# Kernel optimization log

Measured on AMD Instinct MI355X. Metric: run time of the kernel, lower is better.

## Reference

```python
import jax, jax.numpy as jnp
import numpy as np

B, T, N_EMBD, N_HEAD, HEAD_DIM = 4, 2048, 32, 8, 4


def rxtx_blocks(X):
    """Vectorized faithful port of rxtx_4x4 over blocks. X: [..., 4, 4] -> C: [..., 4, 4].
    Computes clip(X) @ clip(X)^T via the 26-multiplication RXTX formulas, except the
    (0,0) and (3,3) entries are 0 (the source sets s1..s8 = 0). Output clipped to [-100,100]."""
    X = jnp.clip(X, -100.0, 100.0)
    (X1, X2, X3, X4) = (X[..., 0, 0], X[..., 0, 1], X[..., 0, 2], X[..., 0, 3])
    (X5, X6, X7, X8) = (X[..., 1, 0], X[..., 1, 1], X[..., 1, 2], X[..., 1, 3])
    (X9, X10, X11, X12) = (X[..., 2, 0], X[..., 2, 1], X[..., 2, 2], X[..., 2, 3])
    (X13, X14, X15, X16) = (X[..., 3, 0], X[..., 3, 1], X[..., 3, 2], X[..., 3, 3])
    m1 = (-X2 + X3 - X4 + X8) * (X8 + X11)
    m2 = (X1 - X5 - X6 + X7) * (X15 + X5)
    m3 = (-X2 + X12) * (-X10 + X16 + X12)
    m4 = (X9 - X6) * (X13 + X9 - X14)
    m5 = (X2 + X11) * (-X6 + X15 - X7)
    m6 = (X6 + X11) * (X6 + X7 - X11)
    m7 = X11 * (X6 + X7)
    m8 = X2 * (-X14 - X10 + X6 - X15 + X7 + X16 + X12)
    m9 = X6 * (X13 + X9 - X14 - X10 + X6 + X7 - X11)
    m10 = (X2 - X3 + X7 + X11 + X4 - X8) * X11
    m11 = (X5 + X6 - X7) * X5
    m12 = (X2 - X3 + X4) * X8
    m13 = (-X1 + X5 + X6 + X3 - X7 + X11) * X15
    m14 = (-X1 + X5 + X6) * (X13 + X9 + X15)
    m15 = (X2 + X4 - X8) * (X11 + X16 + X12)
    m16 = (X1 - X8) * (X9 - X16)
    m17 = X12 * (X10 - X12)
    m18 = X9 * (X13 - X14)
    m19 = (-X2 + X3) * (-X15 + X7 + X8)
    m20 = (X5 + X9 - X8) * X9
    m21 = X8 * (X9 - X8 + X12)
    m22 = (-X6 + X7) * (X5 + X7 - X11)
    m23 = X1 * (X13 - X5 + X16)
    m24 = (-X1 + X4 + X12) * X16
    m25 = (X9 + X2 + X10) * X14
    m26 = (X6 + X10 + X12) * X10
    z1 = m7 - m11 - m12
    z2 = m1 + m12 + m21
    z3 = m3 + m17 - m24
    z4 = m2 + m11 + m23
    z5 = m5 + m7 + m8
    z6 = m4 - m18 - m20
    z7 = m6 - m7 - m9
    z8 = m17 + m18
    c01 = m2 - m5 - z1 + m13 + m19
    c02 = z2 + z3 + m15 + m16
    c03 = z4 - z3 - z5 - m13
    c11 = m1 + m6 - z1 + m10 + m22
    c12 = z2 - z6 + z7 + m10
    c13 = z4 + z6 + m14 + m16
    c22 = m4 - z7 - z8 + m26
    c23 = m3 + z5 + z8 + m25
    zero = jnp.zeros_like(X1)  # s1..s8 = 0 in the source -> corner diagonals are 0
    row0 = jnp.stack([zero, c01, c02, c03], axis=-1)
    row1 = jnp.stack([c01, c11, c12, c13], axis=-1)
    row2 = jnp.stack([c02, c12, c22, c23], axis=-1)
    row3 = jnp.stack([c03, c13, c23, zero], axis=-1)
    C = jnp.stack([row0, row1, row2, row3], axis=-2)
    return jnp.clip(C, -100.0, 100.0)


def setup_inputs() -> dict:
    key = jax.random.key(0)
    ks = jax.random.split(key, 9)
    w_std = 0.02  # ~ xavier_uniform with gain=0.1 for 32x32
    x = jax.random.normal(ks[0], (B, T, N_EMBD), dtype=jnp.float32)
    Wq = jax.random.normal(ks[1], (N_EMBD, N_EMBD), dtype=jnp.float32) * w_std
    Wk = jax.random.normal(ks[2], (N_EMBD, N_EMBD), dtype=jnp.float32) * w_std
    Wv = jax.random.normal(ks[3], (N_EMBD, N_EMBD), dtype=jnp.float32) * w_std
    Wp = jax.random.normal(ks[4], (N_EMBD, N_EMBD), dtype=jnp.float32) * w_std
    bq = jnp.zeros((N_EMBD,), jnp.float32)
    bk = jnp.zeros((N_EMBD,), jnp.float32)
    bv = jnp.zeros((N_EMBD,), jnp.float32)
    bp = jnp.zeros((N_EMBD,), jnp.float32)
    return {"x": x, "Wq": Wq, "bq": bq, "Wk": Wk, "bk": bk, "Wv": Wv, "bv": bv, "Wp": Wp, "bp": bp}


def reference(x, Wq, bq, Wk, bk, Wv, bv, Wp, bp):
    Bx, Tx, Cx = x.shape  # T divisible by 4 -> no padding branch
    H, hd = N_HEAD, HEAD_DIM
    q = (x @ Wq.T + bq).reshape(Bx, Tx, H, hd).transpose(0, 2, 1, 3)  # [B,H,T,4]
    k = (x @ Wk.T + bk)  # computed in the original module but never used in scores
    v = (x @ Wv.T + bv).reshape(Bx, Tx, H, hd).transpose(0, 2, 1, 3)  # [B,H,T,4]
    nb = Tx // 4
    Cb = rxtx_blocks(q.reshape(Bx, H, nb, 4, 4))  # [B,H,nb,4,4]
    # scores[b,h, i*4+r, j*4+c] = Cb[b,h,i,r,c] for every j (source ignores k_block)
    scores = jnp.broadcast_to(Cb[:, :, :, :, None, :], (Bx, H, nb, 4, nb, 4)).reshape(Bx, H, Tx, Tx)
    scores = jnp.clip(scores, -100.0, 100.0) / jnp.sqrt(jnp.float32(hd))
    attn = jax.nn.softmax(scores, axis=-1)  # dropout is identity in eval mode
    out = jnp.einsum('bhts,bhsd->bhtd', attn, v)
    out = out.transpose(0, 2, 1, 3).reshape(Bx, Tx, Cx)
    return out @ Wp.T + bp
```

## Files before the change

### kernel.cpp

```cpp
#include <hip/hip_runtime.h>
#include <math.h>

#define TT 2048
#define CE 32

__device__ __forceinline__ float clip100(float v) {
    return fminf(fmaxf(v, -100.f), 100.f);
}

__device__ __forceinline__ float4 shfl_xor4(float4 v, int m) {
    float4 r;
    r.x = __shfl_xor(v.x, m, 64);
    r.y = __shfl_xor(v.y, m, 64);
    r.z = __shfl_xor(v.z, m, 64);
    r.w = __shfl_xor(v.w, m, 64);
    return r;
}

__global__ __launch_bounds__(512, 2) void k_fused(const float* __restrict__ x,
        const float* __restrict__ Wq, const float* __restrict__ bq,
        const float* __restrict__ Wv, const float* __restrict__ bv,
        const float* __restrict__ Wp, const float* __restrict__ bp,
        float* __restrict__ out) {
    int blk = blockIdx.x;
    int b   = blk >> 6;
    int t0  = (blk & 63) * 32;
    int tid = threadIdx.x;
    int tl  = tid >> 4;
    int h   = (tid >> 1) & 7;
    int s   = tid & 1;

    __shared__ float xs[32][33];
    __shared__ float wqs[32][33];
    __shared__ float wvs[32][33];
    __shared__ float wps[32][33];
    __shared__ float pbuf[32][36];
    __shared__ float Zl[32][36];
    __shared__ float xavg[4][33];
    __shared__ float4 red4[16][32];
    __shared__ float bqs[32], bvs[32], bps[32];

    if (tid < 256) {
        int rr = tid >> 3, cq = tid & 7;
        *reinterpret_cast<float4*>(&wqs[rr][cq * 4]) =
            *reinterpret_cast<const float4*>(Wq + rr * 32 + cq * 4);
        *reinterpret_cast<float4*>(&wvs[rr][cq * 4]) =
            *reinterpret_cast<const float4*>(Wv + rr * 32 + cq * 4);
        *reinterpret_cast<float4*>(&wps[rr][cq * 4]) =
            *reinterpret_cast<const float4*>(Wp + rr * 32 + cq * 4);
    } else {
        int u = tid - 256;
        int r2 = u >> 3, q2 = u & 7;
        *reinterpret_cast<float4*>(&xs[r2][q2 * 4]) =
            *reinterpret_cast<const float4*>(x + ((size_t)b * TT + t0 + r2) * CE + q2 * 4);
        if (u < 32)      bqs[u] = bq[u];
        else if (u < 64) bvs[u - 32] = bv[u - 32];
        else if (u < 96) bps[u - 64] = bp[u - 64];
    }

    {
        const float4* xb4 = reinterpret_cast<const float4*>(x + (size_t)b * TT * CE);
        float4 acc; acc.x = 0.f; acc.y = 0.f; acc.z = 0.f; acc.w = 0.f;
#pragma unroll 8
        for (int it = 0; it < 32; ++it) {
            float4 v = xb4[tid + 512 * it];
            acc.x += v.x; acc.y += v.y; acc.z += v.z; acc.w += v.w;
        }
        red4[tid >> 5][tid & 31] = acc;
    }
    __syncthreads();

    if (tid < 128) {
        int c = tid >> 5, e = tid & 31;
        int g = c * 8 + (e >> 2), comp = e & 3;
        float sm = 0.f;
#pragma unroll
        for (int rg = 0; rg < 16; ++rg)
            sm += reinterpret_cast<const float*>(&red4[rg][g])[comp];
        xavg[c][e] = sm * (1.f / 512.f);
    }

    float4 myq;
    {
        float a0 = 0.f, a1 = 0.f, a2 = 0.f, a3 = 0.f;
#pragma unroll
        for (int e4 = 0; e4 < 4; ++e4) {
            int e = s * 16 + e4 * 4;
            float4 xv = *reinterpret_cast<const float4*>(&xs[tl][e]);
            float4 w0 = *reinterpret_cast<const float4*>(&wqs[4 * h + 0][e]);
            float4 w1 = *reinterpret_cast<const float4*>(&wqs[4 * h + 1][e]);
            float4 w2 = *reinterpret_cast<const float4*>(&wqs[4 * h + 2][e]);
            float4 w3 = *reinterpret_cast<const float4*>(&wqs[4 * h + 3][e]);
            a0 += xv.x * w0.x + xv.y * w0.y + xv.z * w0.z + xv.w * w0.w;
            a1 += xv.x * w1.x + xv.y * w1.y + xv.z * w1.z + xv.w * w1.w;
            a2 += xv.x * w2.x + xv.y * w2.y + xv.z * w2.z + xv.w * w2.w;
            a3 += xv.x * w3.x + xv.y * w3.y + xv.z * w3.z + xv.w * w3.w;
        }
        myq.x = clip100(bqs[4 * h + 0] + a0 + __shfl_xor(a0, 1, 64));
        myq.y = clip100(bqs[4 * h + 1] + a1 + __shfl_xor(a1, 1, 64));
        myq.z = clip100(bqs[4 * h + 2] + a2 + __shfl_xor(a2, 1, 64));
        myq.w = clip100(bqs[4 * h + 3] + a3 + __shfl_xor(a3, 1, 64));
    }

    {
        int r = tl & 3;
        float4 q16 = shfl_xor4(myq, 16);
        float4 q32 = shfl_xor4(myq, 32);
        float4 q48 = shfl_xor4(myq, 48);
        float4 R0 = (r == 0) ? myq : (r == 1) ? q16 : (r == 2) ? q32 : q48;
        float4 R1 = (r == 1) ? myq : (r == 0) ? q16 : (r == 3) ? q32 : q48;
        float4 R2 = (r == 2) ? myq : (r == 3) ? q16 : (r == 0) ? q32 : q48;
        float4 R3 = (r == 3) ? myq : (r == 2) ? q16 : (r == 1) ? q32 : q48;

        float X1 = R0.x, X2 = R0.y, X3 = R0.z, X4 = R0.w;
        float X5 = R1.x, X6 = R1.y, X7 = R1.z, X8 = R1.w;
        float X9 = R2.x, X10 = R2.y, X11 = R2.z, X12 = R2.w;
        float X13 = R3.x, X14 = R3.y, X15 = R3.z, X16 = R3.w;

        float m1  = (-X2 + X3 - X4 + X8) * (X8 + X11);
        float m2  = (X1 - X5 - X6 + X7) * (X15 + X5);
        float m3  = (-X2 + X12) * (-X10 + X16 + X12);
        float m4  = (X9 - X6) * (X13 + X9 - X14);
        float m5  = (X2 + X11) * (-X6 + X15 - X7);
        float m6  = (X6 + X11) * (X6 + X7 - X11);
        float m7  = X11 * (X6 + X7);
        float m8  = X2 * (-X14 - X10 + X6 - X15 + X7 + X16 + X12);
        float m9  = X6 * (X13 + X9 - X14 - X10 + X6 + X7 - X11);
        float m10 = (X2 - X3 + X7 + X11 + X4 - X8) * X11;
        float m11 = (X5 + X6 - X7) * X5;
        float m12 = (X2 - X3 + X4) * X8;
        float m13 = (-X1 + X5 + X6 + X3 - X7 + X11) * X15;
        float m14 = (-X1 + X5 + X6) * (X13 + X9 + X15);
        float m15 = (X2 + X4 - X8) * (X11 + X16 + X12);
        float m16 = (X1 - X8) * (X9 - X16);
        float m17 = X12 * (X10 - X12);
        float m18 = X9 * (X13 - X14);
        float m19 = (-X2 + X3) * (-X15 + X7 + X8);
        float m20 = (X5 + X9 - X8) * X9;
        float m21 = X8 * (X9 - X8 + X12);
        float m22 = (-X6 + X7) * (X5 + X7 - X11);
        float m23 = X1 * (X13 - X5 + X16);
        float m24 = (-X1 + X4 + X12) * X16;
        float m25 = (X9 + X2 + X10) * X14;
        float m26 = (X6 + X10 + X12) * X10;
        float z1 = m7 - m11 - m12;
        float z2 = m1 + m12 + m21;
        float z3 = m3 + m17 - m24;
        float z4 = m2 + m11 + m23;
        float z5 = m5 + m7 + m8;
        float z6 = m4 - m18 - m20;
        float z7 = m6 - m7 - m9;
        float z8 = m17 + m18;
        float c01 = m2 - m5 - z1 + m13 + m19;
        float c02 = z2 + z3 + m15 + m16;
        float c03 = z4 - z3 - z5 - m13;
        float c11 = m1 + m6 - z1 + m10 + m22;
        float c12 = z2 - z6 + z7 + m10;
        float c13 = z4 + z6 + m14 + m16;
        float c22 = m4 - z7 - z8 + m26;
        float c23 = m3 + z5 + z8 + m25;

        float g0, g1, g2, g3;
        if (r == 0)      { g0 = 0.f; g1 = c01; g2 = c02; g3 = c03; }
        else if (r == 1) { g0 = c01; g1 = c11; g2 = c12; g3 = c13; }
        else if (r == 2) { g0 = c02; g1 = c12; g2 = c22; g3 = c23; }
        else             { g0 = c03; g1 = c13; g2 = c23; g3 = 0.f; }
        g0 = clip100(g0) * 0.5f; g1 = clip100(g1) * 0.5f;
        g2 = clip100(g2) * 0.5f; g3 = clip100(g3) * 0.5f;

        float mx = fmaxf(fmaxf(g0, g1), fmaxf(g2, g3));
        float p0 = __expf(g0 - mx), p1 = __expf(g1 - mx);
        float p2 = __expf(g2 - mx), p3 = __expf(g3 - mx);
        float inv = 1.f / (p0 + p1 + p2 + p3);
        if (s == 0) {
            float4 pv; pv.x = p0 * inv; pv.y = p1 * inv;
            pv.z = p2 * inv; pv.w = p3 * inv;
            *reinterpret_cast<float4*>(&pbuf[tl][4 * h]) = pv;
        }
    }
    __syncthreads();

    {
        int k  = tid >> 4;
        int oq = (tid >> 1) & 7;
        int sh = tid & 1;
        int h2 = k >> 2, c2 = k & 3;
        float vv0 = 0.f, vv1 = 0.f, vv2 = 0.f, vv3 = 0.f;
#pragma unroll
        for (int e4 = 0; e4 < 4; ++e4) {
            int e = sh * 16 + e4 * 4;
            float xa0 = xavg[c2][e + 0];
            float xa1 = xavg[c2][e + 1];
            float xa2 = xavg[c2][e + 2];
            float xa3 = xavg[c2][e + 3];
            float4 w0 = *reinterpret_cast<const float4*>(&wvs[4 * h2 + 0][e]);
            float4 w1 = *reinterpret_cast<const float4*>(&wvs[4 * h2 + 1][e]);
            float4 w2 = *reinterpret_cast<const float4*>(&wvs[4 * h2 + 2][e]);
            float4 w3 = *reinterpret_cast<const float4*>(&wvs[4 * h2 + 3][e]);
            vv0 += xa0 * w0.x + xa1 * w0.y + xa2 * w0.z + xa3 * w0.w;
            vv1 += xa0 * w1.x + xa1 * w1.y + xa2 * w1.z + xa3 * w1.w;
            vv2 += xa0 * w2.x + xa1 * w2.y + xa2 * w2.z + xa3 * w2.w;
            vv3 += xa0 * w3.x + xa1 * w3.y + xa2 * w3.z + xa3 * w3.w;
        }
        vv0 = bvs[4 * h2 + 0] + vv0 + __shfl_xor(vv0, 1, 64);
        vv1 = bvs[4 * h2 + 1] + vv1 + __shfl_xor(vv1, 1, 64);
        vv2 = bvs[4 * h2 + 2] + vv2 + __shfl_xor(vv2, 1, 64);
        vv3 = bvs[4 * h2 + 3] + vv3 + __shfl_xor(vv3, 1, 64);
        float zz[2];
#pragma unroll
        for (int dd2 = 0; dd2 < 2; ++dd2) {
            int dd = 2 * sh + dd2;
            float4 wp = *reinterpret_cast<const float4*>(&wps[4 * oq + dd][4 * h2]);
            zz[dd2] = vv0 * wp.x + vv1 * wp.y + vv2 * wp.z + vv3 * wp.w;
        }
        float2 z2v; z2v.x = zz[0]; z2v.y = zz[1];
        *reinterpret_cast<float2*>(&Zl[k][4 * oq + 2 * sh]) = z2v;
    }
    __syncthreads();

    {
        int j = h;
        float o0 = 0.f, o1 = 0.f, o2 = 0.f, o3 = 0.f;
#pragma unroll
        for (int k4 = 0; k4 < 4; ++k4) {
            float4 pv = *reinterpret_cast<const float4*>(&pbuf[tl][16 * s + 4 * k4]);
#pragma unroll
            for (int kk = 0; kk < 4; ++kk) {
                float p = ((const float*)&pv)[kk];
                float4 zv = *reinterpret_cast<const float4*>(&Zl[16 * s + 4 * k4 + kk][4 * j]);
                o0 += p * zv.x; o1 += p * zv.y; o2 += p * zv.z; o3 += p * zv.w;
            }
        }
        o0 += __shfl_xor(o0, 1, 64); o1 += __shfl_xor(o1, 1, 64);
        o2 += __shfl_xor(o2, 1, 64); o3 += __shfl_xor(o3, 1, 64);
        if (s == 0) {
            float4 ov;
            ov.x = bps[4 * j + 0] + o0; ov.y = bps[4 * j + 1] + o1;
            ov.z = bps[4 * j + 2] + o2; ov.w = bps[4 * j + 3] + o3;
            float* orow = out + ((size_t)b * TT + t0 + tl) * CE;
            *reinterpret_cast<float4*>(orow + 4 * j) = ov;
        }
    }
}

extern "C" void kernel_launch(void* const* d_in, const int* in_sizes, int n_in,
                              void* d_out, int out_size, void* d_ws, size_t ws_size,
                              hipStream_t stream) {
    const float* x  = (const float*)d_in[0];
    const float* Wq = (const float*)d_in[1];
    const float* bq = (const float*)d_in[2];
    const float* Wv = (const float*)d_in[5];
    const float* bv = (const float*)d_in[6];
    const float* Wp = (const float*)d_in[7];
    const float* bp = (const float*)d_in[8];
    float* out = (float*)d_out;

    hipLaunchKernelGGL(k_fused, dim3(256), dim3(512), 0, stream,
                       x, Wq, bq, Wv, bv, Wp, bp, out);
}
```

Baseline: 12.39 us.

## Split warps: half reduce column means while other half computes q and softmax

Threads are specialized by role. Threads 256-511 now run the full batch-sum reduction over x, with twice as many iterations each. Threads 0-255 compute the q projection without a pair split (one thread per row-head), then the RXTX scores and softmax, with the shuffle offsets changed to match the new lane mapping. The goal is to overlap the memory-bound reduction with the compute-bound q/softmax stage. The cost is an extra __syncthreads and a longer serial load loop per reducing thread.

```diff
diff --git a/kernel.cpp b/kernel.cpp
--- a/kernel.cpp
+++ b/kernel.cpp
@@ -26,9 +26,6 @@
     int b   = blk >> 6;
     int t0  = (blk & 63) * 32;
     int tid = threadIdx.x;
-    int tl  = tid >> 4;
-    int h   = (tid >> 1) & 7;
-    int s   = tid & 1;
 
     __shared__ float xs[32][33];
     __shared__ float wqs[32][33];
@@ -37,7 +34,7 @@
     __shared__ float pbuf[32][36];
     __shared__ float Zl[32][36];
     __shared__ float xavg[4][33];
-    __shared__ float4 red4[16][32];
+    __shared__ float4 red4[8][32];
     __shared__ float bqs[32], bvs[32], bps[32];
 
     if (tid < 256) {
@@ -48,69 +45,55 @@
             *reinterpret_cast<const float4*>(Wv + rr * 32 + cq * 4);
         *reinterpret_cast<float4*>(&wps[rr][cq * 4]) =
             *reinterpret_cast<const float4*>(Wp + rr * 32 + cq * 4);
+        if (tid < 32)       bqs[tid] = bq[tid];
+        else if (tid < 64)  bvs[tid - 32] = bv[tid - 32];
+        else if (tid < 96)  bps[tid - 64] = bp[tid - 64];
     } else {
         int u = tid - 256;
         int r2 = u >> 3, q2 = u & 7;
         *reinterpret_cast<float4*>(&xs[r2][q2 * 4]) =
             *reinterpret_cast<const float4*>(x + ((size_t)b * TT + t0 + r2) * CE + q2 * 4);
-        if (u < 32)      bqs[u] = bq[u];
-        else if (u < 64) bvs[u - 32] = bv[u - 32];
-        else if (u < 96) bps[u - 64] = bp[u - 64];
-    }
-
-    {
+    }
+    __syncthreads();
+
+    if (tid >= 256) {
+        int u = tid - 256;
         const float4* xb4 = reinterpret_cast<const float4*>(x + (size_t)b * TT * CE);
         float4 acc; acc.x = 0.f; acc.y = 0.f; acc.z = 0.f; acc.w = 0.f;
-#pragma unroll 8
-        for (int it = 0; it < 32; ++it) {
-            float4 v = xb4[tid + 512 * it];
+#pragma unroll 16
+        for (int it = 0; it < 64; ++it) {
+            float4 v = xb4[u + 256 * it];
             acc.x += v.x; acc.y += v.y; acc.z += v.z; acc.w += v.w;
         }
-        red4[tid >> 5][tid & 31] = acc;
-    }
-    __syncthreads();
-
-    if (tid < 128) {
-        int c = tid >> 5, e = tid & 31;
-        int g = c * 8 + (e >> 2), comp = e & 3;
-        float sm = 0.f;
-#pragma unroll
-        for (int rg = 0; rg < 16; ++rg)
-            sm += reinterpret_cast<const float*>(&red4[rg][g])[comp];
-        xavg[c][e] = sm * (1.f / 512.f);
-    }
-
-    float4 myq;
-    {
-        float a0 = 0.f, a1 = 0.f, a2 = 0.f, a3 = 0.f;
-#pragma unroll
-        for (int e4 = 0; e4 < 4; ++e4) {
-            int e = s * 16 + e4 * 4;
-            float4 xv = *reinterpret_cast<const float4*>(&xs[tl][e]);
-            float4 w0 = *reinterpret_cast<const float4*>(&wqs[4 * h + 0][e]);
-            float4 w1 = *reinterpret_cast<const float4*>(&wqs[4 * h + 1][e]);
-            float4 w2 = *reinterpret_cast<const float4*>(&wqs[4 * h + 2][e]);
-            float4 w3 = *reinterpret_cast<const float4*>(&wqs[4 * h + 3][e]);
+        red4[u >> 5][u & 31] = acc;
+    } else {
+        int tl = tid >> 3, h = tid & 7;
+        float a0 = bqs[4 * h + 0], a1 = bqs[4 * h + 1];
+        float a2 = bqs[4 * h + 2], a3 = bqs[4 * h + 3];
+#pragma unroll
+        for (int e4 = 0; e4 < 8; ++e4) {
+            float4 xv = *reinterpret_cast<const float4*>(&xs[tl][e4 * 4]);
+            float4 w0 = *reinterpret_cast<const float4*>(&wqs[4 * h + 0][e4 * 4]);
+            float4 w1 = *reinterpret_cast<const float4*>(&wqs[4 * h + 1][e4 * 4]);
+            float4 w2 = *reinterpret_cast<const float4*>(&wqs[4 * h + 2][e4 * 4]);
+            float4 w3 = *reinterpret_cast<const float4*>(&wqs[4 * h + 3][e4 * 4]);
             a0 += xv.x * w0.x + xv.y * w0.y + xv.z * w0.z + xv.w * w0.w;
             a1 += xv.x * w1.x + xv.y * w1.y + xv.z * w1.z + xv.w * w1.w;
             a2 += xv.x * w2.x + xv.y * w2.y + xv.z * w2.z + xv.w * w2.w;
             a3 += xv.x * w3.x + xv.y * w3.y + xv.z * w3.z + xv.w * w3.w;
         }
-        myq.x = clip100(bqs[4 * h + 0] + a0 + __shfl_xor(a0, 1, 64));
-        myq.y = clip100(bqs[4 * h + 1] + a1 + __shfl_xor(a1, 1, 64));
-        myq.z = clip100(bqs[4 * h + 2] + a2 + __shfl_xor(a2, 1, 64));
-        myq.w = clip100(bqs[4 * h + 3] + a3 + __shfl_xor(a3, 1, 64));
-    }
-
-    {
+        float4 myq;
+        myq.x = clip100(a0); myq.y = clip100(a1);
+        myq.z = clip100(a2); myq.w = clip100(a3);
+
         int r = tl & 3;
+        float4 q8  = shfl_xor4(myq, 8);
         float4 q16 = shfl_xor4(myq, 16);
-        float4 q32 = shfl_xor4(myq, 32);
-        float4 q48 = shfl_xor4(myq, 48);
-        float4 R0 = (r == 0) ? myq : (r == 1) ? q16 : (r == 2) ? q32 : q48;
-        float4 R1 = (r == 1) ? myq : (r == 0) ? q16 : (r == 3) ? q32 : q48;
-        float4 R2 = (r == 2) ? myq : (r == 3) ? q16 : (r == 0) ? q32 : q48;
-        float4 R3 = (r == 3) ? myq : (r == 2) ? q16 : (r == 1) ? q32 : q48;
+        float4 q24 = shfl_xor4(myq, 24);
+        float4 R0 = (r == 0) ? myq : (r == 1) ? q8 : (r == 2) ? q16 : q24;
+        float4 R1 = (r == 1) ? myq : (r == 0) ? q8 : (r == 3) ? q16 : q24;
+        float4 R2 = (r == 2) ? myq : (r == 3) ? q8 : (r == 0) ? q16 : q24;
+        float4 R3 = (r == 3) ? myq : (r == 2) ? q8 : (r == 1) ? q16 : q24;
 
         float X1 = R0.x, X2 = R0.y, X3 = R0.z, X4 = R0.w;
         float X5 = R1.x, X6 = R1.y, X7 = R1.z, X8 = R1.w;
@@ -172,11 +155,20 @@
         float p0 = __expf(g0 - mx), p1 = __expf(g1 - mx);
         float p2 = __expf(g2 - mx), p3 = __expf(g3 - mx);
         float inv = 1.f / (p0 + p1 + p2 + p3);
-        if (s == 0) {
-            float4 pv; pv.x = p0 * inv; pv.y = p1 * inv;
-            pv.z = p2 * inv; pv.w = p3 * inv;
-            *reinterpret_cast<float4*>(&pbuf[tl][4 * h]) = pv;
-        }
+        float4 pv; pv.x = p0 * inv; pv.y = p1 * inv;
+        pv.z = p2 * inv; pv.w = p3 * inv;
+        *reinterpret_cast<float4*>(&pbuf[tl][4 * h]) = pv;
+    }
+    __syncthreads();
+
+    if (tid < 128) {
+        int c = tid >> 5, e = tid & 31;
+        int g = c * 8 + (e >> 2), comp = e & 3;
+        float sm = 0.f;
+#pragma unroll
+        for (int rg = 0; rg < 8; ++rg)
+            sm += reinterpret_cast<const float*>(&red4[rg][g])[comp];
+        xavg[c][e] = sm * (1.f / 512.f);
     }
     __syncthreads();
 
@@ -219,7 +211,7 @@
     __syncthreads();
 
     {
-        int j = h;
+        int tl = tid >> 4, j = (tid >> 1) & 7, s = tid & 1;
         float o0 = 0.f, o1 = 0.f, o2 = 0.f, o3 = 0.f;
 #pragma unroll
         for (int k4 = 0; k4 < 4; ++k4) {
```

Measured after the change: 11.45 us. 1.08x faster.
